# Optimization experiments

Hardware: AMD Instinct MI355X
Metric: run time of the kernel (lower is better)

Reference implementation:

```python
import jax, jax.numpy as jnp
from jax import lax
import numpy as np

IMG=384; PS=16; CIN=3; DIM=512; DEPTH=8; NST=32; HD=64; EXP=2; NC=2; BATCH=32
DIN=EXP*DIM; NH=DIN//HD; CONV_DIM=DIN+2*NST; DPROJ=2*DIN+2*NST+NH
L=(IMG//PS)**2; RD=NST//2; KC=4; EPS=1e-6

# positional RoPE tables for the first RD state dims of B and C
_inv=1.0/(10000.0**(np.arange(0,RD,2)/RD))
_ang=np.arange(L)[:,None]*_inv[None,:]
COS=jnp.asarray(np.cos(_ang),jnp.float32); SIN=jnp.asarray(np.sin(_ang),jnp.float32)

def _rope(v):
    h1=v[...,:RD//2]; h2=v[...,RD//2:RD]
    return jnp.concatenate([h1*COS-h2*SIN, h1*SIN+h2*COS, v[...,RD:]],-1)

def _ln(x,w,b):
    m=jnp.mean(x,-1,keepdims=True); v=jnp.mean((x-m)**2,-1,keepdims=True)
    return (x-m)*lax.rsqrt(v+EPS)*w+b

def _block(x,p):
    ln_w,ln_b,Wp,cw,cb,dtb,Alog,Dsk,Bb,Cb,gw,Wo=p
    B=x.shape[0]
    h=_ln(x,ln_w,ln_b)
    zxbcdt=jnp.einsum('bld,dk->blk',h,Wp)
    z=zxbcdt[...,:DIN]; xBC=zxbcdt[...,DIN:DIN+CONV_DIM]; dt=zxbcdt[...,DIN+CONV_DIM:]
    # causal depthwise conv over sequence
    xc=jnp.pad(xBC.transpose(0,2,1),((0,0),(0,0),(KC-1,0)))
    xc=lax.conv_general_dilated(xc,cw[:,None,:],(1,),'VALID',feature_group_count=CONV_DIM,dimension_numbers=('NCH','OIH','NCH'))
    xBC=jax.nn.silu(xc.transpose(0,2,1)+cb)
    xs=xBC[...,:DIN]; Bm=_rope(xBC[...,DIN:DIN+NST]+Bb); Cm=_rope(xBC[...,DIN+NST:]+Cb)
    dt=jax.nn.softplus(dt+dtb)                       # (B,L,NH)
    dec=jnp.exp(dt*(-jnp.exp(Alog)))                 # (B,L,NH) per-head decay
    xh=xs.reshape(B,L,NH,HD)
    def step(hst,inp):
        d_t,x_t,B_t,C_t,a_t=inp                      # (B,NH),(B,NH,HD),(B,NST),(B,NST),(B,NH)
        hst=a_t[...,None,None]*hst+(d_t[...,None]*x_t)[...,None]*B_t[:,None,None,:]
        return hst,jnp.einsum('bhpn,bn->bhp',hst,C_t)
    h0=jnp.zeros((B,NH,HD,NST),x.dtype)
    seq=(dt.swapaxes(0,1),xh.swapaxes(0,1),Bm.swapaxes(0,1),Cm.swapaxes(0,1),dec.swapaxes(0,1))
    _,ys=lax.scan(step,h0,seq)                       # (L,B,NH,HD)
    y=ys.swapaxes(0,1)+Dsk[None,None,:,None]*xh
    y=y.reshape(B,L,DIN)*jax.nn.silu(z)              # gated RMSNorm
    y=y*lax.rsqrt(jnp.mean(y*y,-1,keepdims=True)+EPS)*gw
    return x+jnp.einsum('bld,dk->blk',y,Wo)

def setup_inputs() -> dict:
    key=jax.random.key(0); ks=jax.random.split(key,12)
    def n(k,sh,s=0.02): return jax.random.normal(k,sh,jnp.float32)*s
    dt0=jnp.exp(jax.random.uniform(ks[5],(DEPTH,NH))*(np.log(0.1)-np.log(0.001))+np.log(0.001))
    return {
        'x': jax.random.normal(ks[0],(BATCH,CIN,IMG,IMG),jnp.float32),
        'patch_w': n(ks[1],(DIM,CIN,PS,PS)), 'patch_b': jnp.zeros((DIM,),jnp.float32),
        'pos_embed': n(ks[2],(1,L,DIM)),
        'ln_w': jnp.ones((DEPTH,DIM),jnp.float32), 'ln_b': jnp.zeros((DEPTH,DIM),jnp.float32),
        'in_proj_w': n(ks[3],(DEPTH,DIM,DPROJ)),
        'conv_w': n(ks[4],(DEPTH,CONV_DIM,KC),0.1), 'conv_b': jnp.zeros((DEPTH,CONV_DIM),jnp.float32),
        'dt_bias': dt0+jnp.log(-jnp.expm1(-dt0)),
        'A_log': jnp.log(1.0+jax.random.uniform(ks[6],(DEPTH,NH))*15.0),
        'D_skip': jnp.ones((DEPTH,NH),jnp.float32),
        'B_bias': jnp.zeros((DEPTH,NST),jnp.float32), 'C_bias': jnp.zeros((DEPTH,NST),jnp.float32),
        'gn_w': jnp.ones((DEPTH,DIN),jnp.float32),
        'out_proj_w': n(ks[7],(DEPTH,DIN,DIM)),
        'norm_w': jnp.ones((DIM,),jnp.float32), 'norm_b': jnp.zeros((DIM,),jnp.float32),
        'head_w': n(ks[8],(DIM,NC)), 'head_b': jnp.zeros((NC,),jnp.float32),
    }

def reference(x,patch_w,patch_b,pos_embed,ln_w,ln_b,in_proj_w,conv_w,conv_b,dt_bias,A_log,D_skip,B_bias,C_bias,gn_w,out_proj_w,norm_w,norm_b,head_w,head_b):
    t=lax.conv_general_dilated(x,patch_w,(PS,PS),'VALID',dimension_numbers=('NCHW','OIHW','NCHW'))+patch_b[None,:,None,None]
    t=t.reshape(t.shape[0],DIM,L).transpose(0,2,1)+pos_embed   # (B,L,DIM)
    params=(ln_w,ln_b,in_proj_w,conv_w,conv_b,dt_bias,A_log,D_skip,B_bias,C_bias,gn_w,out_proj_w)
    t,_=lax.scan(lambda c,p:(_block(c,p),None),t,params)
    t=_ln(t,norm_w,norm_b).mean(1)
    return t@head_w+head_b
```

## Files before the change

### kernel.cpp

```cpp
#include <hip/hip_runtime.h>
#include <cmath>

#define L_TOK 576
#define DIMM  512
#define DINN  1024
#define NHH   16
#define HDD   64
#define NSTT  32
#define CONVD 1088
#define DPROJJ 2128
#define BATCHH 32
#define ROWS  (BATCHH * L_TOK)
#define NPAD  2176
#define NCH   9

typedef unsigned int uint;
typedef __attribute__((ext_vector_type(8))) short bf16x8;
typedef __attribute__((ext_vector_type(4))) float f32x4;

__device__ __forceinline__ float b2f(unsigned short u) {
    union { uint i; float f; } v; v.i = ((uint)u) << 16; return v.f;
}
__device__ __forceinline__ unsigned short f2b(float x) {
    union { float f; uint i; } v; v.f = x;
    uint r = (v.i + 0x7FFFu + ((v.i >> 16) & 1u)) >> 16;
    return (unsigned short)r;
}

__device__ __forceinline__ void gload16(const unsigned short* g, unsigned short* lds) {
    __builtin_amdgcn_global_load_lds(
        (const __attribute__((address_space(1))) unsigned int*)g,
        (__attribute__((address_space(3))) unsigned int*)lds, 16, 0, 0);
}

__device__ __forceinline__ int swz64(int row, int col) {
    return row * 128 + ((((col >> 3) ^ row) & 7) << 4) + (col & 7) * 2;
}

__global__ void rope_init(float* __restrict__ COS, float* __restrict__ SIN) {
    int i = blockIdx.x * 256 + threadIdx.x;
    if (i >= L_TOK * 8) return;
    int l = i >> 3, j = i & 7;
    double inv = pow(10000.0, -(double)(2 * j) / 16.0);
    double a = (double)l * inv;
    COS[i] = (float)cos(a);
    SIN[i] = (float)sin(a);
}

__global__ __launch_bounds__(256) void transpose_pad(
        const float* __restrict__ src, unsigned short* __restrict__ dst,
        int R, int C, int Cp) {
    __shared__ float tile[32][33];
    int lz = blockIdx.z;
    const float* S = src + (size_t)lz * R * C;
    unsigned short* D = dst + (size_t)lz * Cp * R;
    int c0 = blockIdx.x * 32, r0 = blockIdx.y * 32;
    int tx = threadIdx.x & 31, ty = threadIdx.x >> 5;
#pragma unroll
    for (int i = 0; i < 32; i += 8) {
        int c = c0 + tx;
        tile[ty + i][tx] = (c < C) ? S[(size_t)(r0 + ty + i) * C + c] : 0.f;
    }
    __syncthreads();
#pragma unroll
    for (int i = 0; i < 32; i += 8) {
        int cc = c0 + ty + i;
        int rr = r0 + tx;
        if (cc < Cp) D[(size_t)cc * R + rr] = f2b(tile[tx][ty + i]);
    }
}

__global__ void f32tobf16_kernel(const float* __restrict__ src, unsigned short* __restrict__ dst,
                                 int n) {
    int i = blockIdx.x * 256 + threadIdx.x;
    if (i < n) dst[i] = f2b(src[i]);
}

__global__ __launch_bounds__(192) void im2col_kernel(
        const float* __restrict__ img, unsigned short* __restrict__ A) {
    int m = blockIdx.x;
    int tid = threadIdx.x;
    int b = m / L_TOK, l = m % L_TOK;
    int oy = l / 24, ox = l % 24;
    int k = tid * 4;
    int c = k >> 8, rem = k & 255, iy = rem >> 4, ix = rem & 15;
    const float* p = img + ((size_t)(b * 3 + c) * 384 + oy * 16 + iy) * 384 + ox * 16 + ix;
    float4 v = *(const float4*)p;
    ushort4 u;
    u.x = f2b(v.x); u.y = f2b(v.y); u.z = f2b(v.z); u.w = f2b(v.w);
    *(ushort4*)(A + (size_t)m * 768 + k) = u;
}

__global__ __launch_bounds__(256) void gemm_patch_mfma(
        const unsigned short* __restrict__ A, const unsigned short* __restrict__ Bt,
        const float* __restrict__ pb, const float* __restrict__ pos,
        float* __restrict__ X) {
    __shared__ unsigned short As[128 * 64];
    __shared__ unsigned short Bs[128 * 64];
    const int tid = threadIdx.x;
    const int l = tid & 63, w = tid >> 6;
    const int wr = w >> 1, wc = w & 1;
    const int m0 = blockIdx.y * 128, n0 = blockIdx.x * 128;
    f32x4 acc[4][4];
#pragma unroll
    for (int i = 0; i < 4; ++i)
#pragma unroll
        for (int j = 0; j < 4; ++j) acc[i][j] = (f32x4)(0.f);

    int rA[4], rB[4];
#pragma unroll
    for (int f = 0; f < 4; ++f) {
        rA[f] = wr * 64 + f * 16 + (l & 15);
        rB[f] = wc * 64 + f * 16 + (l & 15);
    }
    const char* AsB = (const char*)As;
    const char* BsB = (const char*)Bs;

    for (int k0 = 0; k0 < 768; k0 += 64) {
        __syncthreads();
#pragma unroll
        for (int i = 0; i < 4; ++i) {
            int lin = i * 256 + tid;
            int r = lin >> 3, slot = lin & 7;
            int sc = (slot ^ (r & 7)) * 8;
            gload16(A  + (size_t)(m0 + r) * 768 + k0 + sc, As + lin * 8);
            gload16(Bt + (size_t)(n0 + r) * 768 + k0 + sc, Bs + lin * 8);
        }
        __syncthreads();
#pragma unroll
        for (int kk = 0; kk < 2; ++kk) {
            bf16x8 af[4], bfr[4];
            int c16 = kk * 4 + (l >> 4);
#pragma unroll
            for (int f = 0; f < 4; ++f) {
                int row = rA[f];
                af[f] = *(const bf16x8*)(AsB + row * 128 + ((c16 ^ (row & 7)) << 4));
            }
#pragma unroll
            for (int f = 0; f < 4; ++f) {
                int row = rB[f];
                bfr[f] = *(const bf16x8*)(BsB + row * 128 + ((c16 ^ (row & 7)) << 4));
            }
#pragma unroll
            for (int mf = 0; mf < 4; ++mf)
#pragma unroll
                for (int nf = 0; nf < 4; ++nf)
                    acc[mf][nf] = __builtin_amdgcn_mfma_f32_16x16x32_bf16(
                        af[mf], bfr[nf], acc[mf][nf], 0, 0, 0);
        }
    }
#pragma unroll
    for (int mf = 0; mf < 4; ++mf)
#pragma unroll
        for (int nf = 0; nf < 4; ++nf) {
            int col = n0 + wc * 64 + nf * 16 + (l & 15);
            float pbv = pb[col];
#pragma unroll
            for (int reg = 0; reg < 4; ++reg) {
                int row = m0 + wr * 64 + mf * 16 + (l >> 4) * 4 + reg;
                int tokl = row % L_TOK;
                X[(size_t)row * DIMM + col] =
                    acc[mf][nf][reg] + pbv + pos[(size_t)tokl * DIMM + col];
            }
        }
}

__global__ __launch_bounds__(256) void lnbf16_kernel(
        const float* __restrict__ X, const float* __restrict__ w,
        const float* __restrict__ bi, unsigned short* __restrict__ Hb) {
    int row = blockIdx.x * 4 + (threadIdx.x >> 6);
    int lane = threadIdx.x & 63;
    const float* xr = X + (size_t)row * DIMM;
    float4 u0 = *(const float4*)(xr + lane * 8);
    float4 u1 = *(const float4*)(xr + lane * 8 + 4);
    float v[8] = {u0.x, u0.y, u0.z, u0.w, u1.x, u1.y, u1.z, u1.w};
    float s = 0.f;
#pragma unroll
    for (int j = 0; j < 8; ++j) s += v[j];
#pragma unroll
    for (int o = 32; o > 0; o >>= 1) s += __shfl_xor(s, o);
    float m = s * (1.f / DIMM);
    float q = 0.f;
#pragma unroll
    for (int j = 0; j < 8; ++j) { float d = v[j] - m; q += d * d; }
#pragma unroll
    for (int o = 32; o > 0; o >>= 1) q += __shfl_xor(q, o);
    float rstd = rsqrtf(q * (1.f / DIMM) + 1e-6f);
    float4 w0 = *(const float4*)(w + lane * 8);
    float4 w1 = *(const float4*)(w + lane * 8 + 4);
    float4 b0 = *(const float4*)(bi + lane * 8);
    float4 b1 = *(const float4*)(bi + lane * 8 + 4);
    float wv[8] = {w0.x, w0.y, w0.z, w0.w, w1.x, w1.y, w1.z, w1.w};
    float bv[8] = {b0.x, b0.y, b0.z, b0.w, b1.x, b1.y, b1.z, b1.w};
    ushort4 s0, s1;
    s0.x = f2b((v[0] - m) * rstd * wv[0] + bv[0]);
    s0.y = f2b((v[1] - m) * rstd * wv[1] + bv[1]);
    s0.z = f2b((v[2] - m) * rstd * wv[2] + bv[2]);
    s0.w = f2b((v[3] - m) * rstd * wv[3] + bv[3]);
    s1.x = f2b((v[4] - m) * rstd * wv[4] + bv[4]);
    s1.y = f2b((v[5] - m) * rstd * wv[5] + bv[5]);
    s1.z = f2b((v[6] - m) * rstd * wv[6] + bv[6]);
    s1.w = f2b((v[7] - m) * rstd * wv[7] + bv[7]);
    unsigned short* orow = Hb + (size_t)row * DIMM + lane * 8;
    *(ushort4*)(orow) = s0;
    *(ushort4*)(orow + 4) = s1;
}

__global__ __launch_bounds__(256) void rowstat_kernel(
        const float* __restrict__ X, float* __restrict__ RS) {
    int row = blockIdx.x * 4 + (threadIdx.x >> 6);
    int lane = threadIdx.x & 63;
    const float* xr = X + (size_t)row * DIMM;
    float4 u0 = *(const float4*)(xr + lane * 8);
    float4 u1 = *(const float4*)(xr + lane * 8 + 4);
    float v[8] = {u0.x, u0.y, u0.z, u0.w, u1.x, u1.y, u1.z, u1.w};
    float s = 0.f;
#pragma unroll
    for (int j = 0; j < 8; ++j) s += v[j];
#pragma unroll
    for (int o = 32; o > 0; o >>= 1) s += __shfl_xor(s, o);
    float m = s * (1.f / DIMM);
    float q = 0.f;
#pragma unroll
    for (int j = 0; j < 8; ++j) { float d = v[j] - m; q += d * d; }
#pragma unroll
    for (int o = 32; o > 0; o >>= 1) q += __shfl_xor(q, o);
    float rstd = rsqrtf(q * (1.f / DIMM) + 1e-6f);
    if (lane == 0) {
        RS[row * 2 + 0] = m;
        RS[row * 2 + 1] = rstd;
    }
}

__global__ __launch_bounds__(256) void gemm_in_mfma(
        const unsigned short* __restrict__ A,
        const unsigned short* __restrict__ Bt,
        unsigned short* __restrict__ Z, unsigned short* __restrict__ XBC,
        float* __restrict__ DTRAW) {
    __shared__ unsigned short As[128 * 64];
    __shared__ unsigned short Bs[128 * 64];
    const int tid = threadIdx.x;
    const int l = tid & 63, w = tid >> 6;
    const int wr = w >> 1, wc = w & 1;
    const int m0 = blockIdx.y * 128, n0 = blockIdx.x * 128;
    f32x4 acc[4][4];
#pragma unroll
    for (int i = 0; i < 4; ++i)
#pragma unroll
        for (int j = 0; j < 4; ++j) acc[i][j] = (f32x4)(0.f);

    int rA[4], rB[4];
#pragma unroll
    for (int f = 0; f < 4; ++f) {
        rA[f] = wr * 64 + f * 16 + (l & 15);
        rB[f] = wc * 64 + f * 16 + (l & 15);
    }
    const char* AsB = (const char*)As;
    const char* BsB = (const char*)Bs;

    for (int k0 = 0; k0 < 512; k0 += 64) {
        __syncthreads();
#pragma unroll
        for (int i = 0; i < 4; ++i) {
            int lin = i * 256 + tid;
            int r = lin >> 3, slot = lin & 7;
            int sc = (slot ^ (r & 7)) * 8;
            gload16(A  + (size_t)(m0 + r) * 512 + k0 + sc, As + lin * 8);
            gload16(Bt + (size_t)(n0 + r) * 512 + k0 + sc, Bs + lin * 8);
        }
        __syncthreads();
#pragma unroll
        for (int kk = 0; kk < 2; ++kk) {
            bf16x8 af[4], bfr[4];
            int c16 = kk * 4 + (l >> 4);
#pragma unroll
            for (int f = 0; f < 4; ++f) {
                int row = rA[f];
                af[f] = *(const bf16x8*)(AsB + row * 128 + ((c16 ^ (row & 7)) << 4));
            }
#pragma unroll
            for (int f = 0; f < 4; ++f) {
                int row = rB[f];
                bfr[f] = *(const bf16x8*)(BsB + row * 128 + ((c16 ^ (row & 7)) << 4));
            }
#pragma unroll
            for (int mf = 0; mf < 4; ++mf)
#pragma unroll
                for (int nf = 0; nf < 4; ++nf)
                    acc[mf][nf] = __builtin_amdgcn_mfma_f32_16x16x32_bf16(
                        af[mf], bfr[nf], acc[mf][nf], 0, 0, 0);
        }
    }
#pragma unroll
    for (int mf = 0; mf < 4; ++mf)
#pragma unroll
        for (int nf = 0; nf < 4; ++nf) {
            int col = n0 + wc * 64 + nf * 16 + (l & 15);
#pragma unroll
            for (int reg = 0; reg < 4; ++reg) {
                int row = m0 + wr * 64 + mf * 16 + (l >> 4) * 4 + reg;
                float v = acc[mf][nf][reg];
                if (col < DINN)             Z[(size_t)row * DINN + col] = f2b(v);
                else if (col < DINN + CONVD) XBC[(size_t)row * CONVD + (col - DINN)] = f2b(v);
                else if (col < DPROJJ)       DTRAW[(size_t)row * NHH + (col - DINN - CONVD)] = v;
            }
        }
}

__global__ __launch_bounds__(256) void gemm_out_mfma(
        const unsigned short* __restrict__ A,
        const unsigned short* __restrict__ Bt,
        float* __restrict__ X) {
    __shared__ unsigned short As[128 * 64];
    __shared__ unsigned short Bs[128 * 64];
    const int tid = threadIdx.x;
    const int l = tid & 63, w = tid >> 6;
    const int wr = w >> 1, wc = w & 1;
    const int m0 = blockIdx.y * 128, n0 = blockIdx.x * 128;
    f32x4 acc[4][4];
#pragma unroll
    for (int i = 0; i < 4; ++i)
#pragma unroll
        for (int j = 0; j < 4; ++j) acc[i][j] = (f32x4)(0.f);

    int rA[4], rB[4];
#pragma unroll
    for (int f = 0; f < 4; ++f) {
        rA[f] = wr * 64 + f * 16 + (l & 15);
        rB[f] = wc * 64 + f * 16 + (l & 15);
    }
    const char* AsB = (const char*)As;
    const char* BsB = (const char*)Bs;

    for (int k0 = 0; k0 < 1024; k0 += 64) {
        __syncthreads();
#pragma unroll
        for (int i = 0; i < 4; ++i) {
            int lin = i * 256 + tid;
            int r = lin >> 3, slot = lin & 7;
            int sc = (slot ^ (r & 7)) * 8;
            gload16(A  + (size_t)(m0 + r) * 1024 + k0 + sc, As + lin * 8);
            gload16(Bt + (size_t)(n0 + r) * 1024 + k0 + sc, Bs + lin * 8);
        }
        __syncthreads();
#pragma unroll
        for (int kk = 0; kk < 2; ++kk) {
            bf16x8 af[4], bfr[4];
            int c16 = kk * 4 + (l >> 4);
#pragma unroll
            for (int f = 0; f < 4; ++f) {
                int row = rA[f];
                af[f] = *(const bf16x8*)(AsB + row * 128 + ((c16 ^ (row & 7)) << 4));
            }
#pragma unroll
            for (int f = 0; f < 4; ++f) {
                int row = rB[f];
                bfr[f] = *(const bf16x8*)(BsB + row * 128 + ((c16 ^ (row & 7)) << 4));
            }
#pragma unroll
            for (int mf = 0; mf < 4; ++mf)
#pragma unroll
                for (int nf = 0; nf < 4; ++nf)
                    acc[mf][nf] = __builtin_amdgcn_mfma_f32_16x16x32_bf16(
                        af[mf], bfr[nf], acc[mf][nf], 0, 0, 0);
        }
    }
#pragma unroll
    for (int mf = 0; mf < 4; ++mf)
#pragma unroll
        for (int nf = 0; nf < 4; ++nf) {
            int col = n0 + wc * 64 + nf * 16 + (l & 15);
#pragma unroll
            for (int reg = 0; reg < 4; ++reg) {
                int row = m0 + wr * 64 + mf * 16 + (l >> 4) * 4 + reg;
                float* p = X + (size_t)row * DIMM + col;
                *p += acc[mf][nf][reg];
            }
        }
}

__global__ __launch_bounds__(256) void conv_kernel(
        const unsigned short* __restrict__ XBC, const float* __restrict__ cw,
        const float* __restrict__ cb,
        const float* __restrict__ Bb, const float* __restrict__ Cb,
        const float* __restrict__ COS, const float* __restrict__ SIN,
        unsigned short* __restrict__ XS, float* __restrict__ BM, float* __restrict__ CM) {
    __shared__ unsigned short sh[35][128];
    int tileIdx = blockIdx.x;
    int c0 = blockIdx.y * 128;
    int b = tileIdx / 18, lt = tileIdx % 18;
    int l0 = lt * 32;
    int r0 = b * L_TOK + l0;

    for (int idx = threadIdx.x; idx < 35 * 128; idx += 256) {
        int row = idx >> 7, col = idx & 127;
        int t = l0 - 3 + row;
        int c = c0 + col;
        unsigned short v = 0;
        if (t >= 0 && c < CONVD)
            v = XBC[(size_t)(b * L_TOK + t) * CONVD + c];
        sh[row][col] = v;
    }
    __syncthreads();

    int tx = threadIdx.x & 127, ty = threadIdx.x >> 7;
    int c = c0 + tx;
    if (c >= CONVD) return;
    float w0 = cw[c * 4 + 0], w1 = cw[c * 4 + 1], w2 = cw[c * 4 + 2], w3 = cw[c * 4 + 3];
    float bias = cb[c];

    if (c < DINN) {
#pragma unroll
        for (int i = 0; i < 16; ++i) {
            int t = ty * 16 + i;
            float acc = w0 * b2f(sh[t][tx]) + w1 * b2f(sh[t + 1][tx])
                      + w2 * b2f(sh[t + 2][tx]) + w3 * b2f(sh[t + 3][tx]);
            float v = acc + bias;
            v = v / (1.f + expf(-v));
            XS[(size_t)(r0 + t) * DINN + c] = f2b(v);
        }
    } else {
        int j = c - DINN;
        int jj = j & 31;
        bool isB = j < 32;
        float bias2 = isB ? Bb[jj] : Cb[jj];
        int i0 = jj & 7;
#pragma unroll
        for (int i = 0; i < 16; ++i) {
            int t = ty * 16 + i;
            int lglob = l0 + t;
            float acc = w0 * b2f(sh[t][tx]) + w1 * b2f(sh[t + 1][tx])
                      + w2 * b2f(sh[t + 2][tx]) + w3 * b2f(sh[t + 3][tx]);
            float v = acc + bias;
            v = v / (1.f + expf(-v));
            float v2 = v + bias2;
            float partner = __shfl_xor(v2, 8);
            float outv;
            if (jj < 16) {
                float cs = COS[lglob * 8 + i0], sn = SIN[lglob * 8 + i0];
                outv = (jj < 8) ? (v2 * cs - partner * sn) : (partner * sn + v2 * cs);
            } else {
                outv = v2;
            }
            if (isB) BM[(size_t)(r0 + t) * NSTT + jj] = outv;
            else     CM[(size_t)(r0 + t) * NSTT + jj] = outv;
        }
    }
}

__global__ __launch_bounds__(64) void scanA_kernel(
        unsigned short* __restrict__ XSY,
        const float* __restrict__ DTRAW, const float* __restrict__ dtb,
        const float* __restrict__ Alog,
        const float* __restrict__ BM, const float* __restrict__ CM,
        const float* __restrict__ Dsk,
        float* __restrict__ SC, float* __restrict__ ET, float* __restrict__ ECH) {
    int c = blockIdx.x, bh = blockIdx.y;
    int b = bh >> 4, h = bh & 15;
    int l = threadIdx.x;
    int r0 = b * L_TOK + c * 64;

    __shared__ unsigned short Wl[64 * 64];
    __shared__ unsigned short XT[64 * 64];
    __shared__ unsigned short BT[32 * 64];
    __shared__ float Lsh[64];
    __shared__ float dtsh[64];

    float raw = DTRAW[(size_t)(r0 + l) * NHH + h] + dtb[h];
    float dtl = fmaxf(raw, 0.f) + log1pf(expf(-fabsf(raw)));
    float L = -expf(Alog[h]) * dtl;
#pragma unroll
    for (int off = 1; off < 64; off <<= 1) {
        float v = __shfl_up(L, off);
        if (l >= off) L += v;
    }
    float LEND = __shfl(L, 63);
    ET[(size_t)bh * L_TOK + c * 64 + l] = __expf(L);
    if (l == 0) ECH[bh * NCH + c] = __expf(LEND);
    Lsh[l] = L;
    dtsh[l] = dtl;
    float ul = __expf(LEND - L) * dtl;
    float dsk = Dsk[h];

    bf16x8 cf[4], bq[4];
#pragma unroll
    for (int f = 0; f < 4; ++f) {
        const float* cp = CM + (size_t)(r0 + f * 16 + (l & 15)) * NSTT + (l >> 4) * 8;
        const float* bp = BM + (size_t)(r0 + f * 16 + (l & 15)) * NSTT + (l >> 4) * 8;
        float4 c0 = *(const float4*)cp, c1 = *(const float4*)(cp + 4);
        float4 b0 = *(const float4*)bp, b1 = *(const float4*)(bp + 4);
        bf16x8 cv, bv;
        cv[0]=(short)f2b(c0.x); cv[1]=(short)f2b(c0.y); cv[2]=(short)f2b(c0.z); cv[3]=(short)f2b(c0.w);
        cv[4]=(short)f2b(c1.x); cv[5]=(short)f2b(c1.y); cv[6]=(short)f2b(c1.z); cv[7]=(short)f2b(c1.w);
        bv[0]=(short)f2b(b0.x); bv[1]=(short)f2b(b0.y); bv[2]=(short)f2b(b0.z); bv[3]=(short)f2b(b0.w);
        bv[4]=(short)f2b(b1.x); bv[5]=(short)f2b(b1.y); bv[6]=(short)f2b(b1.z); bv[7]=(short)f2b(b1.w);
        cf[f] = cv; bq[f] = bv;
    }
    f32x4 acc[4][4];
#pragma unroll
    for (int i = 0; i < 4; ++i)
#pragma unroll
        for (int j = 0; j < 4; ++j) acc[i][j] = (f32x4)(0.f);
#pragma unroll
    for (int mf = 0; mf < 4; ++mf)
#pragma unroll
        for (int nf = 0; nf < 4; ++nf)
            acc[mf][nf] = __builtin_amdgcn_mfma_f32_16x16x32_bf16(cf[mf], bq[nf], acc[mf][nf], 0, 0, 0);

    __builtin_amdgcn_wave_barrier();
#pragma unroll
    for (int nf = 0; nf < 4; ++nf) {
        int s = nf * 16 + (l & 15);
        float Ls = Lsh[s], dts = dtsh[s];
#pragma unroll
        for (int mf = 0; mf < 4; ++mf) {
#pragma unroll
            for (int reg = 0; reg < 4; ++reg) {
                int t = mf * 16 + (l >> 4) * 4 + reg;
                float Lt = Lsh[t];
                float v = acc[mf][nf][reg];
                float wv = (s <= t) ? __expf(Lt - Ls) * dts * v : 0.f;
                if (s == t) wv += dsk;
                *(unsigned short*)((char*)Wl + swz64(t, s)) = f2b(wv);
            }
        }
    }

    uint xw[32];
    {
        const uint* xp = (const uint*)(XSY + (size_t)(r0 + l) * DINN + h * HDD);
#pragma unroll
        for (int i = 0; i < 8; ++i) {
            uint4 v = *(const uint4*)(xp + i * 4);
            xw[i*4+0]=v.x; xw[i*4+1]=v.y; xw[i*4+2]=v.z; xw[i*4+3]=v.w;
        }
    }
#pragma unroll
    for (int p = 0; p < 64; ++p) {
        unsigned short xv = (p & 1) ? (unsigned short)(xw[p >> 1] >> 16)
                                    : (unsigned short)(xw[p >> 1] & 0xffffu);
        *(unsigned short*)((char*)XT + swz64(p, l)) = xv;
    }
    __builtin_amdgcn_wave_barrier();

    f32x4 yacc[4][4];
#pragma unroll
    for (int i = 0; i < 4; ++i)
#pragma unroll
        for (int j = 0; j < 4; ++j) yacc[i][j] = (f32x4)(0.f);
#pragma unroll
    for (int kk = 0; kk < 2; ++kk) {
        int slot = kk * 4 + (l >> 4);
        bf16x8 wf[4], xf[4];
#pragma unroll
        for (int f = 0; f < 4; ++f) {
            int rw = f * 16 + (l & 15);
            wf[f] = *(const bf16x8*)((const char*)Wl + rw * 128 + (((slot ^ rw) & 7) << 4));
            xf[f] = *(const bf16x8*)((const char*)XT + rw * 128 + (((slot ^ rw) & 7) << 4));
        }
#pragma unroll
        for (int mf = 0; mf < 4; ++mf)
#pragma unroll
            for (int nf = 0; nf < 4; ++nf)
                yacc[mf][nf] = __builtin_amdgcn_mfma_f32_16x16x32_bf16(
                    wf[mf], xf[nf], yacc[mf][nf], 0, 0, 0);
    }

    __builtin_amdgcn_wave_barrier();
#pragma unroll
    for (int mf = 0; mf < 4; ++mf)
#pragma unroll
        for (int nf = 0; nf < 4; ++nf)
#pragma unroll
            for (int reg = 0; reg < 4; ++reg) {
                int t = mf * 16 + (l >> 4) * 4 + reg;
                int p = nf * 16 + (l & 15);
                *(unsigned short*)((char*)Wl + swz64(t, p)) = f2b(yacc[mf][nf][reg]);
            }
    __builtin_amdgcn_wave_barrier();
    {
        unsigned short* yp = XSY + (size_t)(r0 + l) * DINN + h * HDD;
#pragma unroll
        for (int j = 0; j < 8; ++j) {
            uint4 v = *(const uint4*)((const char*)Wl + l * 128 + (((j ^ l) & 7) << 4));
            *(uint4*)(yp + j * 8) = v;
        }
    }

    __builtin_amdgcn_wave_barrier();
#pragma unroll
    for (int p = 0; p < 64; ++p) {
        unsigned short xv = (p & 1) ? (unsigned short)(xw[p >> 1] >> 16)
                                    : (unsigned short)(xw[p >> 1] & 0xffffu);
        *(unsigned short*)((char*)XT + swz64(p, l)) = f2b(b2f(xv) * ul);
    }
    {
        const float* bp = BM + (size_t)(r0 + l) * NSTT;
#pragma unroll
        for (int n = 0; n < 32; n += 4) {
            float4 v = *(const float4*)(bp + n);
            *(unsigned short*)((char*)BT + swz64(n + 0, l)) = f2b(v.x);
            *(unsigned short*)((char*)BT + swz64(n + 1, l)) = f2b(v.y);
            *(unsigned short*)((char*)BT + swz64(n + 2, l)) = f2b(v.z);
            *(unsigned short*)((char*)BT + swz64(n + 3, l)) = f2b(v.w);
        }
    }
    __builtin_amdgcn_wave_barrier();
    f32x4 sacc[4][2];
#pragma unroll
    for (int i = 0; i < 4; ++i)
#pragma unroll
        for (int j = 0; j < 2; ++j) sacc[i][j] = (f32x4)(0.f);
#pragma unroll
    for (int kk = 0; kk < 2; ++kk) {
        int slot = kk * 4 + (l >> 4);
        bf16x8 uf[4], btf[2];
#pragma unroll
        for (int f = 0; f < 4; ++f) {
            int rw = f * 16 + (l & 15);
            uf[f] = *(const bf16x8*)((const char*)XT + rw * 128 + (((slot ^ rw) & 7) << 4));
        }
#pragma unroll
        for (int f = 0; f < 2; ++f) {
            int rw = f * 16 + (l & 15);
            btf[f] = *(const bf16x8*)((const char*)BT + rw * 128 + (((slot ^ rw) & 7) << 4));
        }
#pragma unroll
        for (int mf = 0; mf < 4; ++mf)
#pragma unroll
            for (int nf = 0; nf < 2; ++nf)
                sacc[mf][nf] = __builtin_amdgcn_mfma_f32_16x16x32_bf16(
                    uf[mf], btf[nf], sacc[mf][nf], 0, 0, 0);
    }
    {
        float* sp = SC + (size_t)(bh * NCH + c) * 64 * 32;
#pragma unroll
        for (int mf = 0; mf < 4; ++mf)
#pragma unroll
            for (int nf = 0; nf < 2; ++nf)
#pragma unroll
                for (int reg = 0; reg < 4; ++reg) {
                    int p = mf * 16 + (l >> 4) * 4 + reg;
                    int n = nf * 16 + (l & 15);
                    sp[p * 32 + n] = sacc[mf][nf][reg];
                }
    }
}

__global__ __launch_bounds__(64) void scanB_kernel(
        float* __restrict__ SC, const float* __restrict__ ECH) {
    int bh = blockIdx.x;
    int p = threadIdx.x;
    float H[32];
#pragma unroll
    for (int n = 0; n < 32; ++n) H[n] = 0.f;
    for (int c = 0; c < NCH; ++c) {
        float e = ECH[bh * NCH + c];
        float* sp = SC + ((size_t)(bh * NCH + c) * 64 + p) * 32;
        float s[32];
#pragma unroll
        for (int n4 = 0; n4 < 8; ++n4) {
            float4 v = *(const float4*)(sp + n4 * 4);
            s[n4*4+0]=v.x; s[n4*4+1]=v.y; s[n4*4+2]=v.z; s[n4*4+3]=v.w;
        }
#pragma unroll
        for (int n4 = 0; n4 < 8; ++n4)
            *(float4*)(sp + n4 * 4) = make_float4(H[n4*4+0], H[n4*4+1], H[n4*4+2], H[n4*4+3]);
#pragma unroll
        for (int n = 0; n < 32; ++n) H[n] = e * H[n] + s[n];
    }
}

__global__ __launch_bounds__(64) void scanC_kernel(
        unsigned short* __restrict__ XSY, const float* __restrict__ SC,
        const float* __restrict__ CM, const float* __restrict__ ET) {
    int c = blockIdx.x, bh = blockIdx.y;
    int b = bh >> 4, h = bh & 15;
    int l = threadIdx.x;
    int r0 = b * L_TOK + c * 64;
    __shared__ float CEsh[64][36];
#pragma unroll
    for (int i = 0; i < 32; ++i) {
        int idx = i * 64 + l;
        int t = idx >> 5, n = idx & 31;
        CEsh[t][n] = CM[(size_t)(r0 + t) * NSTT + n] * ET[(size_t)bh * L_TOK + c * 64 + t];
    }
    const float* hp = SC + ((size_t)(bh * NCH + c) * 64 + l) * 32;
    float H[32];
#pragma unroll
    for (int n4 = 0; n4 < 8; ++n4) {
        float4 v = *(const float4*)(hp + n4 * 4);
        H[n4*4+0]=v.x; H[n4*4+1]=v.y; H[n4*4+2]=v.z; H[n4*4+3]=v.w;
    }
    __builtin_amdgcn_wave_barrier();
    unsigned short* yp = XSY + (size_t)r0 * DINN + h * HDD + l;
    for (int t = 0; t < 64; ++t) {
        float acc = 0.f;
#pragma unroll
        for (int n4 = 0; n4 < 8; ++n4) {
            float4 ce = *(const float4*)&CEsh[t][n4 * 4];
            acc += ce.x * H[n4*4+0] + ce.y * H[n4*4+1]
                 + ce.z * H[n4*4+2] + ce.w * H[n4*4+3];
        }
        float y = b2f(yp[(size_t)t * DINN]) + acc;
        yp[(size_t)t * DINN] = f2b(y);
    }
}

__global__ __launch_bounds__(256) void rmsgate_kernel(
        unsigned short* __restrict__ Y, const unsigned short* __restrict__ Z,
        const float* __restrict__ gw) {
    int row = blockIdx.x * 4 + (threadIdx.x >> 6);
    int lane = threadIdx.x & 63;
    unsigned short* yr = Y + (size_t)row * DINN + lane * 16;
    const unsigned short* zr = Z + (size_t)row * DINN + lane * 16;
    float g[16];
    float q = 0.f;
#pragma unroll
    for (int i = 0; i < 16; ++i) {
        float yv = b2f(yr[i]);
        float zv = b2f(zr[i]);
        float gz = zv / (1.f + expf(-zv));
        g[i] = yv * gz;
        q += g[i] * g[i];
    }
#pragma unroll
    for (int o = 32; o > 0; o >>= 1) q += __shfl_xor(q, o);
    float sc = rsqrtf(q * (1.f / DINN) + 1e-6f);
#pragma unroll
    for (int i = 0; i < 16; ++i) {
        float wv = gw[lane * 16 + i];
        yr[i] = f2b(g[i] * sc * wv);
    }
}

__global__ void lnmean_kernel(const float* __restrict__ X, const float* __restrict__ RS,
                              const float* __restrict__ nw, const float* __restrict__ nb,
                              float* __restrict__ MEAN) {
    int b = blockIdx.x >> 1;
    int d = (blockIdx.x & 1) * 256 + threadIdx.x;
    float w = nw[d], bb = nb[d];
    const float* p = X + (size_t)b * L_TOK * DIMM + d;
    const float* rs = RS + (size_t)b * L_TOK * 2;
    float s = 0.f;
    for (int l = 0; l < L_TOK; ++l) {
        float m = rs[l * 2 + 0], r = rs[l * 2 + 1];
        s += (p[(size_t)l * DIMM] - m) * r * w + bb;
    }
    MEAN[b * DIMM + d] = s * (1.f / L_TOK);
}

__global__ void head_kernel(const float* __restrict__ MEAN, const float* __restrict__ hw,
                            const float* __restrict__ hb, float* __restrict__ out) {
    int t = threadIdx.x;
    if (t >= 64) return;
    int b = t >> 1, c = t & 1;
    float s = 0.f;
    for (int k = 0; k < DIMM; ++k) s += MEAN[b * DIMM + k] * hw[k * 2 + c];
    out[b * 2 + c] = s + hb[c];
}

extern "C" void kernel_launch(void* const* d_in, const int* in_sizes, int n_in,
                              void* d_out, int out_size, void* d_ws, size_t ws_size,
                              hipStream_t stream) {
    const float* x_img   = (const float*)d_in[0];
    const float* patch_w = (const float*)d_in[1];
    const float* patch_b = (const float*)d_in[2];
    const float* pos     = (const float*)d_in[3];
    const float* ln_w    = (const float*)d_in[4];
    const float* ln_b    = (const float*)d_in[5];
    const float* Wp      = (const float*)d_in[6];
    const float* cw      = (const float*)d_in[7];
    const float* cb      = (const float*)d_in[8];
    const float* dtb     = (const float*)d_in[9];
    const float* Alog    = (const float*)d_in[10];
    const float* Dsk     = (const float*)d_in[11];
    const float* Bb      = (const float*)d_in[12];
    const float* Cb      = (const float*)d_in[13];
    const float* gnw     = (const float*)d_in[14];
    const float* Wo      = (const float*)d_in[15];
    const float* nw      = (const float*)d_in[16];
    const float* nb      = (const float*)d_in[17];
    const float* hw      = (const float*)d_in[18];
    const float* hb      = (const float*)d_in[19];
    float* out = (float*)d_out;

    char* base = (char*)d_ws;
    size_t off = 0;
    auto alloc = [&](size_t bytes) -> char* {
        char* p = base + off;
        off += (bytes + 255) & ~(size_t)255;
        return p;
    };
    float*          X     = (float*)alloc((size_t)ROWS * DIMM * 4);
    unsigned short* XBC   = (unsigned short*)alloc((size_t)ROWS * CONVD * 2);
    unsigned short* Z     = (unsigned short*)alloc((size_t)ROWS * DINN * 2);
    unsigned short* XSY   = (unsigned short*)alloc((size_t)ROWS * DINN * 2);
    unsigned short* Hb    = (unsigned short*)alloc((size_t)ROWS * DIMM * 2);
    unsigned short* WpT   = (unsigned short*)alloc((size_t)8 * NPAD * DIMM * 2);
    unsigned short* WoT   = (unsigned short*)alloc((size_t)8 * DIMM * DINN * 2);
    float*          DTRAW = (float*)alloc((size_t)ROWS * NHH * 4);
    float*          BMp   = (float*)alloc((size_t)ROWS * NSTT * 4);
    float*          CMp   = (float*)alloc((size_t)ROWS * NSTT * 4);
    float*          RS    = (float*)alloc((size_t)ROWS * 2 * 4);
    float*          COS   = (float*)alloc((size_t)L_TOK * 8 * 4);
    float*          SIN   = (float*)alloc((size_t)L_TOK * 8 * 4);
    float*          MEAN  = (float*)alloc((size_t)BATCHH * DIMM * 4);
    float*          ET    = (float*)alloc((size_t)BATCHH * NHH * L_TOK * 4);
    float*          ECH   = (float*)alloc((size_t)BATCHH * NHH * NCH * 4);
    unsigned short* AIM   = XBC;
    unsigned short* PWB   = Z;
    float*          SCp   = (float*)XBC;
    if (off > ws_size) return;

    rope_init<<<18, 256, 0, stream>>>(COS, SIN);
    transpose_pad<<<dim3(NPAD / 32, DIMM / 32, 8), 256, 0, stream>>>(Wp, WpT, DIMM, DPROJJ, NPAD);
    transpose_pad<<<dim3(DIMM / 32, DINN / 32, 8), 256, 0, stream>>>(Wo, WoT, DINN, DIMM, DIMM);

    f32tobf16_kernel<<<(512 * 768 + 255) / 256, 256, 0, stream>>>(patch_w, PWB, 512 * 768);
    im2col_kernel<<<ROWS, 192, 0, stream>>>(x_img, AIM);
    gemm_patch_mfma<<<dim3(4, 144), 256, 0, stream>>>(AIM, PWB, patch_b, pos, X);

    for (int i = 0; i < 8; ++i) {
        lnbf16_kernel<<<ROWS / 4, 256, 0, stream>>>(X, ln_w + i * DIMM, ln_b + i * DIMM, Hb);
        gemm_in_mfma<<<dim3(NPAD / 128, ROWS / 128), 256, 0, stream>>>(
            Hb, WpT + (size_t)i * NPAD * DIMM, Z, XBC, DTRAW);
        conv_kernel<<<dim3(BATCHH * 18, 9), 256, 0, stream>>>(
            XBC, cw + (size_t)i * CONVD * 4, cb + (size_t)i * CONVD,
            Bb + i * NSTT, Cb + i * NSTT, COS, SIN, XSY, BMp, CMp);
        scanA_kernel<<<dim3(NCH, BATCHH * NHH), 64, 0, stream>>>(
            XSY, DTRAW, dtb + i * NHH, Alog + i * NHH, BMp, CMp, Dsk + i * NHH, SCp, ET, ECH);
        scanB_kernel<<<BATCHH * NHH, 64, 0, stream>>>(SCp, ECH);
        scanC_kernel<<<dim3(NCH, BATCHH * NHH), 64, 0, stream>>>(XSY, SCp, CMp, ET);
        rmsgate_kernel<<<ROWS / 4, 256, 0, stream>>>(XSY, Z, gnw + (size_t)i * DINN);
        gemm_out_mfma<<<dim3(DIMM / 128, ROWS / 128), 256, 0, stream>>>(
            XSY, WoT + (size_t)i * DIMM * DINN, X);
    }

    rowstat_kernel<<<ROWS / 4, 256, 0, stream>>>(X, RS);
    lnmean_kernel<<<64, 256, 0, stream>>>(X, RS, nw, nb, MEAN);
    head_kernel<<<1, 64, 0, stream>>>(MEAN, hw, hb, out);
}
```

Measured before the change: 2.783 ms.

## Swizzle GEMM block order, stage gemm_in epilogue via LDS, vectorize rmsgate

The three GEMMs now run on a 1D grid whose block index is remapped with an XCD-style swizzle (stride by 8), so blocks sent to the same chiplet work on neighbouring tiles and share L2. The gemm_in epilogue for the Z and XBC tiles writes the bf16 results into shared memory first and then stores them with coalesced 16-byte rows instead of scattered 2-byte writes. rmsgate loads and stores y and z with uint4 vectors. These aim to cut L2 misses and reduce the number of store transactions, at the cost of an extra LDS round trip and syncs in the epilogue.

```diff
diff --git a/kernel.cpp b/kernel.cpp
--- a/kernel.cpp
+++ b/kernel.cpp
@@ -100,7 +100,8 @@
     const int tid = threadIdx.x;
     const int l = tid & 63, w = tid >> 6;
     const int wr = w >> 1, wc = w & 1;
-    const int m0 = blockIdx.y * 128, n0 = blockIdx.x * 128;
+    int swz = (blockIdx.x & 7) * 72 + (blockIdx.x >> 3);
+    const int m0 = (swz >> 2) * 128, n0 = (swz & 3) * 128;
     f32x4 acc[4][4];
 #pragma unroll
     for (int i = 0; i < 4; ++i)
@@ -237,12 +238,15 @@
         const unsigned short* __restrict__ Bt,
         unsigned short* __restrict__ Z, unsigned short* __restrict__ XBC,
         float* __restrict__ DTRAW) {
-    __shared__ unsigned short As[128 * 64];
-    __shared__ unsigned short Bs[128 * 64];
+    __shared__ unsigned short SH[2][128 * 64];
+    unsigned short* As = SH[0];
+    unsigned short* Bs = SH[1];
     const int tid = threadIdx.x;
     const int l = tid & 63, w = tid >> 6;
     const int wr = w >> 1, wc = w & 1;
-    const int m0 = blockIdx.y * 128, n0 = blockIdx.x * 128;
+    int swz = (blockIdx.x & 7) * 306 + (blockIdx.x >> 3);
+    const int nx = swz % 17, my = swz / 17;
+    const int m0 = my * 128, n0 = nx * 128;
     f32x4 acc[4][4];
 #pragma unroll
     for (int i = 0; i < 4; ++i)
@@ -291,20 +295,47 @@
                         af[mf], bfr[nf], acc[mf][nf], 0, 0, 0);
         }
     }
-#pragma unroll
-    for (int mf = 0; mf < 4; ++mf)
-#pragma unroll
-        for (int nf = 0; nf < 4; ++nf) {
-            int col = n0 + wc * 64 + nf * 16 + (l & 15);
-#pragma unroll
-            for (int reg = 0; reg < 4; ++reg) {
-                int row = m0 + wr * 64 + mf * 16 + (l >> 4) * 4 + reg;
-                float v = acc[mf][nf][reg];
-                if (col < DINN)             Z[(size_t)row * DINN + col] = f2b(v);
-                else if (col < DINN + CONVD) XBC[(size_t)row * CONVD + (col - DINN)] = f2b(v);
-                else if (col < DPROJJ)       DTRAW[(size_t)row * NHH + (col - DINN - CONVD)] = v;
-            }
-        }
+
+    if (nx < 16) {
+        __syncthreads();
+        unsigned short* T = &SH[0][0];
+#pragma unroll
+        for (int mf = 0; mf < 4; ++mf)
+#pragma unroll
+            for (int nf = 0; nf < 4; ++nf) {
+                int tcol = wc * 64 + nf * 16 + (l & 15);
+#pragma unroll
+                for (int reg = 0; reg < 4; ++reg) {
+                    int trow = wr * 64 + mf * 16 + (l >> 4) * 4 + reg;
+                    T[trow * 128 + tcol] = f2b(acc[mf][nf][reg]);
+                }
+            }
+        __syncthreads();
+        const bool isZ = n0 < DINN;
+        unsigned short* dbase = isZ ? (Z + n0) : (XBC + (n0 - DINN));
+        const int stride = isZ ? DINN : CONVD;
+#pragma unroll
+        for (int p = 0; p < 8; ++p) {
+            int row = p * 16 + (tid >> 4);
+            uint4 v = *(const uint4*)((const char*)T + row * 256 + (tid & 15) * 16);
+            unsigned short* drow = dbase + (size_t)(m0 + row) * stride;
+            *(uint4*)((char*)drow + (tid & 15) * 16) = v;
+        }
+    } else {
+#pragma unroll
+        for (int mf = 0; mf < 4; ++mf)
+#pragma unroll
+            for (int nf = 0; nf < 4; ++nf) {
+                int col = n0 + wc * 64 + nf * 16 + (l & 15);
+#pragma unroll
+                for (int reg = 0; reg < 4; ++reg) {
+                    int row = m0 + wr * 64 + mf * 16 + (l >> 4) * 4 + reg;
+                    float v = acc[mf][nf][reg];
+                    if (col < DINN + CONVD)  XBC[(size_t)row * CONVD + (col - DINN)] = f2b(v);
+                    else if (col < DPROJJ)   DTRAW[(size_t)row * NHH + (col - DINN - CONVD)] = v;
+                }
+            }
+    }
 }
 
 __global__ __launch_bounds__(256) void gemm_out_mfma(
@@ -316,7 +347,8 @@
     const int tid = threadIdx.x;
     const int l = tid & 63, w = tid >> 6;
     const int wr = w >> 1, wc = w & 1;
-    const int m0 = blockIdx.y * 128, n0 = blockIdx.x * 128;
+    int swz = (blockIdx.x & 7) * 72 + (blockIdx.x >> 3);
+    const int m0 = (swz >> 2) * 128, n0 = (swz & 3) * 128;
     f32x4 acc[4][4];
 #pragma unroll
     for (int i = 0; i < 4; ++i)
@@ -714,24 +746,39 @@
     int lane = threadIdx.x & 63;
     unsigned short* yr = Y + (size_t)row * DINN + lane * 16;
     const unsigned short* zr = Z + (size_t)row * DINN + lane * 16;
+    uint4 y0 = *(const uint4*)yr;
+    uint4 y1 = *(const uint4*)(yr + 8);
+    uint4 z0 = *(const uint4*)zr;
+    uint4 z1 = *(const uint4*)(zr + 8);
+    uint yw[8] = {y0.x, y0.y, y0.z, y0.w, y1.x, y1.y, y1.z, y1.w};
+    uint zw[8] = {z0.x, z0.y, z0.z, z0.w, z1.x, z1.y, z1.z, z1.w};
     float g[16];
     float q = 0.f;
 #pragma unroll
-    for (int i = 0; i < 16; ++i) {
-        float yv = b2f(yr[i]);
-        float zv = b2f(zr[i]);
-        float gz = zv / (1.f + expf(-zv));
-        g[i] = yv * gz;
-        q += g[i] * g[i];
+    for (int i = 0; i < 8; ++i) {
+        float ylo = b2f((unsigned short)(yw[i] & 0xffffu));
+        float yhi = b2f((unsigned short)(yw[i] >> 16));
+        float zlo = b2f((unsigned short)(zw[i] & 0xffffu));
+        float zhi = b2f((unsigned short)(zw[i] >> 16));
+        float glo = ylo * (zlo / (1.f + expf(-zlo)));
+        float ghi = yhi * (zhi / (1.f + expf(-zhi)));
+        g[2*i] = glo; g[2*i+1] = ghi;
+        q += glo * glo + ghi * ghi;
     }
 #pragma unroll
     for (int o = 32; o > 0; o >>= 1) q += __shfl_xor(q, o);
     float sc = rsqrtf(q * (1.f / DINN) + 1e-6f);
-#pragma unroll
-    for (int i = 0; i < 16; ++i) {
-        float wv = gw[lane * 16 + i];
-        yr[i] = f2b(g[i] * sc * wv);
-    }
+    const float* gwp = gw + lane * 16;
+    uint ow[8];
+#pragma unroll
+    for (int i = 0; i < 8; ++i) {
+        float wlo = gwp[2*i], whi = gwp[2*i+1];
+        uint lo = f2b(g[2*i] * sc * wlo);
+        uint hi = f2b(g[2*i+1] * sc * whi);
+        ow[i] = lo | (hi << 16);
+    }
+    *(uint4*)yr = make_uint4(ow[0], ow[1], ow[2], ow[3]);
+    *(uint4*)(yr + 8) = make_uint4(ow[4], ow[5], ow[6], ow[7]);
 }
 
 __global__ void lnmean_kernel(const float* __restrict__ X, const float* __restrict__ RS,
@@ -819,11 +866,11 @@
 
     f32tobf16_kernel<<<(512 * 768 + 255) / 256, 256, 0, stream>>>(patch_w, PWB, 512 * 768);
     im2col_kernel<<<ROWS, 192, 0, stream>>>(x_img, AIM);
-    gemm_patch_mfma<<<dim3(4, 144), 256, 0, stream>>>(AIM, PWB, patch_b, pos, X);
+    gemm_patch_mfma<<<576, 256, 0, stream>>>(AIM, PWB, patch_b, pos, X);
 
     for (int i = 0; i < 8; ++i) {
         lnbf16_kernel<<<ROWS / 4, 256, 0, stream>>>(X, ln_w + i * DIMM, ln_b + i * DIMM, Hb);
-        gemm_in_mfma<<<dim3(NPAD / 128, ROWS / 128), 256, 0, stream>>>(
+        gemm_in_mfma<<<2448, 256, 0, stream>>>(
             Hb, WpT + (size_t)i * NPAD * DIMM, Z, XBC, DTRAW);
         conv_kernel<<<dim3(BATCHH * 18, 9), 256, 0, stream>>>(
             XBC, cw + (size_t)i * CONVD * 4, cb + (size_t)i * CONVD,
@@ -833,7 +880,7 @@
         scanB_kernel<<<BATCHH * NHH, 64, 0, stream>>>(SCp, ECH);
         scanC_kernel<<<dim3(NCH, BATCHH * NHH), 64, 0, stream>>>(XSY, SCp, CMp, ET);
         rmsgate_kernel<<<ROWS / 4, 256, 0, stream>>>(XSY, Z, gnw + (size_t)i * DINN);
-        gemm_out_mfma<<<dim3(DIMM / 128, ROWS / 128), 256, 0, stream>>>(
+        gemm_out_mfma<<<576, 256, 0, stream>>>(
             XSY, WoT + (size_t)i * DIMM * DINN, X);
     }
 
```

After: 2.665 ms. 1.04x faster.
